# Performance work log

Measured on AMD Instinct MI355X. Metric: run time of the kernel, lower is better.

Reference implementation:

```python
import jax, jax.numpy as jnp
import numpy as np

N_NODES = 100000
N_HYPEREDGES = 50000
N_CAND = 200000
SET_SIZE = 8
EMB_DIM = 64


def setup_inputs() -> dict:
    key = jax.random.key(0)
    k1, k2, k3, k4 = jax.random.split(key, 4)
    node_emb = jax.random.normal(k1, (N_NODES, EMB_DIM), dtype=jnp.float32)
    hyperedge_emb = jax.random.normal(k2, (N_HYPEREDGES, EMB_DIM), dtype=jnp.float32)
    h = jax.random.randint(k3, (N_CAND,), 0, N_HYPEREDGES, dtype=jnp.int64)
    X = jax.random.randint(k4, (N_CAND, SET_SIZE), 0, N_NODES, dtype=jnp.int64)
    return {"node_emb": node_emb, "hyperedge_emb": hyperedge_emb, "h": h, "X": X}


def reference(node_emb, hyperedge_emb, h, X):
    # Gather per-candidate embeddings
    src = hyperedge_emb[h]          # [E, d]
    embs = node_emb[X]              # [E, S, d]

    # star_: min over nodes of sigmoid(<hyperedge, node>)
    star_scores = jax.nn.sigmoid(jnp.einsum('ed,esd->es', src, embs))  # [E, S]
    star = jnp.min(star_scores, axis=1, keepdims=True)                 # [E, 1]

    # clique_: min over all pairs of sigmoid(<node_i, node_j>)
    pair_scores = jax.nn.sigmoid(jnp.einsum('esd,etd->est', embs, embs))  # [E, S, S]
    clique = jnp.min(pair_scores, axis=(1, 2), keepdims=False)[:, None]   # [E, 1]

    return jnp.concatenate([star, clique], axis=-1)  # [E, 2]
```

## Files before the change

### kernel.cpp

```cpp
#include <hip/hip_runtime.h>
#include <hip/hip_fp16.h>
#include <math.h>
#include <float.h>

#define SET_SIZE 8
#define EMB_DIM 64
#define NPAIR 36
#define NDOT (SET_SIZE + NPAIR)

typedef _Float16 f16x2 __attribute__((ext_vector_type(2)));

union Frag32 {
    float4 f4[2];
    f16x2  h2[8];
};

__device__ __forceinline__ float dot16_f16(const Frag32& a, const Frag32& b) {
    float c = 0.0f;
#pragma unroll
    for (int j = 0; j < 8; ++j)
        c = __builtin_amdgcn_fdot2(a.h2[j], b.h2[j], c, false);
    return c;
}

__device__ __forceinline__ float quad_reduce_add(float x) {
    int t = __builtin_amdgcn_update_dpp(0, __float_as_int(x), 0xB1, 0xF, 0xF, true);
    x += __int_as_float(t);
    t = __builtin_amdgcn_update_dpp(0, __float_as_int(x), 0x4E, 0xF, 0xF, true);
    x += __int_as_float(t);
    return x;
}

__global__ __launch_bounds__(256) void cvt_both_kernel(
    const float* __restrict__ a, const float* __restrict__ b,
    __half* __restrict__ oa, __half* __restrict__ ob, int n8a, int n8b)
{
    int i = blockIdx.x * blockDim.x + threadIdx.x;
    const float* in;
    __half* out;
    int j;
    if (i < n8a) { in = a; out = oa; j = i; }
    else if (i < n8a + n8b) { in = b; out = ob; j = i - n8a; }
    else return;
    const float4* p = (const float4*)in + 2 * (size_t)j;
    float4 x = p[0], y = p[1];
    union { __half2 h2[4]; float4 f4; } u;
    u.h2[0] = __floats2half2_rn(x.x, x.y);
    u.h2[1] = __floats2half2_rn(x.z, x.w);
    u.h2[2] = __floats2half2_rn(y.x, y.y);
    u.h2[3] = __floats2half2_rn(y.z, y.w);
    ((float4*)out)[j] = u.f4;
}

__global__ __launch_bounds__(256, 5) void hyperedge_score_q4(
    const __half* __restrict__ node_f16,
    const __half* __restrict__ he_f16,
    const int*    __restrict__ h,
    const int*    __restrict__ X,
    float*        __restrict__ out,
    int n_cand)
{
    int tid = blockIdx.x * blockDim.x + threadIdx.x;
    int grp = tid >> 2;
    int q   = tid & 3;
    if (grp >= n_cand) return;

    const int4* Xv = (const int4*)(X + (size_t)grp * SET_SIZE);
    int4 x0 = Xv[0];
    int4 x1 = Xv[1];
    int he = h[grp];
    int idx[SET_SIZE] = {x0.x, x0.y, x0.z, x0.w, x1.x, x1.y, x1.z, x1.w};

    Frag32 v[9];
#pragma unroll
    for (int r = 0; r < SET_SIZE; ++r) {
        const float4* p = (const float4*)(node_f16 + (size_t)idx[r] * EMB_DIM);
        v[r].f4[0] = p[q];
        v[r].f4[1] = p[q + 4];
    }
    {
        const float4* p = (const float4*)(he_f16 + (size_t)he * EMB_DIM);
        v[8].f4[0] = p[q];
        v[8].f4[1] = p[q + 4];
    }

    float smin = FLT_MAX;
#pragma unroll
    for (int s = 0; s < SET_SIZE; ++s) {
        float d = quad_reduce_add(dot16_f16(v[8], v[s]));
        smin = fminf(smin, d);
    }

    float pmin = FLT_MAX;
#pragma unroll
    for (int s = 0; s < SET_SIZE; ++s) {
#pragma unroll
        for (int t = s; t < SET_SIZE; ++t) {
            float d = quad_reduce_add(dot16_f16(v[s], v[t]));
            pmin = fminf(pmin, d);
        }
    }

    float res = (q == 0) ? 1.0f / (1.0f + __expf(-smin))
                         : 1.0f / (1.0f + __expf(-pmin));
    if (q < 2) out[(size_t)grp * 2 + q] = res;
}

__device__ __forceinline__ float dot4f(float4 a, float4 b) {
    return fmaf(a.x, b.x, fmaf(a.y, b.y, fmaf(a.z, b.z, a.w * b.w)));
}

__global__ __launch_bounds__(256) void hyperedge_score_f32(
    const float* __restrict__ node_emb, const float* __restrict__ hyperedge_emb,
    const int* __restrict__ h, const int* __restrict__ X,
    float* __restrict__ out, int n_cand)
{
    int tid = blockIdx.x * blockDim.x + threadIdx.x;
    int grp = tid >> 3;
    int q   = tid & 7;
    if (grp >= n_cand) return;
    const int4* Xv = (const int4*)(X + (size_t)grp * SET_SIZE);
    int4 x0 = Xv[0]; int4 x1 = Xv[1];
    int he = h[grp];
    int idx[SET_SIZE] = {x0.x, x0.y, x0.z, x0.w, x1.x, x1.y, x1.z, x1.w};
    float4 va[9], vb[9];
#pragma unroll
    for (int r = 0; r < SET_SIZE; ++r) {
        const float4* p = (const float4*)(node_emb + (size_t)idx[r] * EMB_DIM) + 2 * q;
        va[r] = p[0]; vb[r] = p[1];
    }
    {
        const float4* p = (const float4*)(hyperedge_emb + (size_t)he * EMB_DIM) + 2 * q;
        va[8] = p[0]; vb[8] = p[1];
    }
    float acc[NDOT];
#pragma unroll
    for (int s = 0; s < SET_SIZE; ++s)
        acc[s] = dot4f(va[8], va[s]) + dot4f(vb[8], vb[s]);
    {
        int k = SET_SIZE;
#pragma unroll
        for (int s = 0; s < SET_SIZE; ++s)
#pragma unroll
            for (int t = s; t < SET_SIZE; ++t, ++k)
                acc[k] = dot4f(va[s], va[t]) + dot4f(vb[s], vb[t]);
    }
#pragma unroll
    for (int i = 0; i < NDOT; ++i) {
        float x = acc[i];
        x += __shfl_xor(x, 1);
        x += __shfl_xor(x, 2);
        x += __shfl_xor(x, 4);
        acc[i] = x;
    }
    float smin = acc[0];
#pragma unroll
    for (int s = 1; s < SET_SIZE; ++s) smin = fminf(smin, acc[s]);
    float pmin = acc[SET_SIZE];
#pragma unroll
    for (int i = 1; i < NPAIR; ++i) pmin = fminf(pmin, acc[SET_SIZE + i]);
    float res = (q == 0) ? 1.0f / (1.0f + __expf(-smin))
                         : 1.0f / (1.0f + __expf(-pmin));
    if (q < 2) out[(size_t)grp * 2 + q] = res;
}

extern "C" void kernel_launch(void* const* d_in, const int* in_sizes, int n_in,
                              void* d_out, int out_size, void* d_ws, size_t ws_size,
                              hipStream_t stream) {
    const float* node_emb      = (const float*)d_in[0];
    const float* hyperedge_emb = (const float*)d_in[1];
    const int*   h             = (const int*)d_in[2];
    const int*   X             = (const int*)d_in[3];
    float*       out           = (float*)d_out;

    int n_node_elems = in_sizes[0];
    int n_he_elems   = in_sizes[1];
    int n_cand       = in_sizes[2];

    size_t need = ((size_t)n_node_elems + (size_t)n_he_elems) * sizeof(__half);
    int block = 256;

    if (ws_size >= need) {
        __half* node_f16 = (__half*)d_ws;
        __half* he_f16   = node_f16 + n_node_elems;

        int n8_node = n_node_elems / 8;
        int n8_he   = n_he_elems / 8;
        int n8_tot  = n8_node + n8_he;
        cvt_both_kernel<<<(n8_tot + block - 1) / block, block, 0, stream>>>(
            node_emb, hyperedge_emb, node_f16, he_f16, n8_node, n8_he);

        long long total_threads = (long long)n_cand * 4;
        int grid_main = (int)((total_threads + block - 1) / block);
        hyperedge_score_q4<<<grid_main, block, 0, stream>>>(
            node_f16, he_f16, h, X, out, n_cand);
    } else {
        long long total_threads = (long long)n_cand * 8;
        int grid_main = (int)((total_threads + block - 1) / block);
        hyperedge_score_f32<<<grid_main, block, 0, stream>>>(
            node_emb, hyperedge_emb, h, X, out, n_cand);
    }
}
```

Before: 114.4 us.

## Grid-stride main kernel with index prefetch and nontemporal loads/stores

Turns the fp16 scoring kernel into a grid-stride loop with half as many threads, each handling two candidates. The next candidate's X and h indices are prefetched while the current one computes. Conversion loads, index loads and output stores use nontemporal hints, and the output is written as one float2 per candidate. The occupancy hint drops from 5 to 4 waves. This trades parallelism (fewer waves in flight to hide the random-gather latency) for less launch and index-fetch latency per candidate. The fp32 fallback is also restructured to reduce each dot immediately instead of keeping an accumulator array.

```diff
diff --git a/kernel.cpp b/kernel.cpp
--- a/kernel.cpp
+++ b/kernel.cpp
@@ -9,6 +9,9 @@
 #define NDOT (SET_SIZE + NPAIR)
 
 typedef _Float16 f16x2 __attribute__((ext_vector_type(2)));
+typedef float    vf4   __attribute__((ext_vector_type(4)));
+typedef float    vf2   __attribute__((ext_vector_type(2)));
+typedef int      vi4   __attribute__((ext_vector_type(4)));
 
 union Frag32 {
     float4 f4[2];
@@ -42,17 +45,18 @@
     if (i < n8a) { in = a; out = oa; j = i; }
     else if (i < n8a + n8b) { in = b; out = ob; j = i - n8a; }
     else return;
-    const float4* p = (const float4*)in + 2 * (size_t)j;
-    float4 x = p[0], y = p[1];
-    union { __half2 h2[4]; float4 f4; } u;
+    const vf4* p = (const vf4*)in + 2 * (size_t)j;
+    vf4 x = __builtin_nontemporal_load(p);
+    vf4 y = __builtin_nontemporal_load(p + 1);
+    union { __half2 h2[4]; vf4 f4; } u;
     u.h2[0] = __floats2half2_rn(x.x, x.y);
     u.h2[1] = __floats2half2_rn(x.z, x.w);
     u.h2[2] = __floats2half2_rn(y.x, y.y);
     u.h2[3] = __floats2half2_rn(y.z, y.w);
-    ((float4*)out)[j] = u.f4;
-}
-
-__global__ __launch_bounds__(256, 5) void hyperedge_score_q4(
+    ((vf4*)out)[j] = u.f4;
+}
+
+__global__ __launch_bounds__(256, 4) void hyperedge_score_q4(
     const __half* __restrict__ node_f16,
     const __half* __restrict__ he_f16,
     const int*    __restrict__ h,
@@ -60,50 +64,68 @@
     float*        __restrict__ out,
     int n_cand)
 {
-    int tid = blockIdx.x * blockDim.x + threadIdx.x;
-    int grp = tid >> 2;
-    int q   = tid & 3;
+    int tid  = blockIdx.x * blockDim.x + threadIdx.x;
+    int grp  = tid >> 2;
+    int q    = tid & 3;
+    int quads = (gridDim.x * blockDim.x) >> 2;
+
     if (grp >= n_cand) return;
 
-    const int4* Xv = (const int4*)(X + (size_t)grp * SET_SIZE);
-    int4 x0 = Xv[0];
-    int4 x1 = Xv[1];
-    int he = h[grp];
-    int idx[SET_SIZE] = {x0.x, x0.y, x0.z, x0.w, x1.x, x1.y, x1.z, x1.w};
-
-    Frag32 v[9];
-#pragma unroll
-    for (int r = 0; r < SET_SIZE; ++r) {
-        const float4* p = (const float4*)(node_f16 + (size_t)idx[r] * EMB_DIM);
-        v[r].f4[0] = p[q];
-        v[r].f4[1] = p[q + 4];
-    }
-    {
-        const float4* p = (const float4*)(he_f16 + (size_t)he * EMB_DIM);
-        v[8].f4[0] = p[q];
-        v[8].f4[1] = p[q + 4];
-    }
-
-    float smin = FLT_MAX;
-#pragma unroll
-    for (int s = 0; s < SET_SIZE; ++s) {
-        float d = quad_reduce_add(dot16_f16(v[8], v[s]));
-        smin = fminf(smin, d);
-    }
-
-    float pmin = FLT_MAX;
-#pragma unroll
-    for (int s = 0; s < SET_SIZE; ++s) {
-#pragma unroll
-        for (int t = s; t < SET_SIZE; ++t) {
-            float d = quad_reduce_add(dot16_f16(v[s], v[t]));
-            pmin = fminf(pmin, d);
-        }
-    }
-
-    float res = (q == 0) ? 1.0f / (1.0f + __expf(-smin))
-                         : 1.0f / (1.0f + __expf(-pmin));
-    if (q < 2) out[(size_t)grp * 2 + q] = res;
+    vi4 nx0 = __builtin_nontemporal_load((const vi4*)(X + (size_t)grp * SET_SIZE));
+    vi4 nx1 = __builtin_nontemporal_load((const vi4*)(X + (size_t)grp * SET_SIZE) + 1);
+    int nhe = h[grp];
+
+    for (int c = grp; c < n_cand; c += quads) {
+        vi4 x0 = nx0, x1 = nx1;
+        int he = nhe;
+        int idx[SET_SIZE] = {x0.x, x0.y, x0.z, x0.w, x1.x, x1.y, x1.z, x1.w};
+
+        Frag32 v[9];
+#pragma unroll
+        for (int r = 0; r < SET_SIZE; ++r) {
+            const float4* p = (const float4*)(node_f16 + (size_t)idx[r] * EMB_DIM);
+            v[r].f4[0] = p[q];
+            v[r].f4[1] = p[q + 4];
+        }
+        {
+            const float4* p = (const float4*)(he_f16 + (size_t)he * EMB_DIM);
+            v[8].f4[0] = p[q];
+            v[8].f4[1] = p[q + 4];
+        }
+
+        int cn = c + quads;
+        if (cn < n_cand) {
+            nx0 = __builtin_nontemporal_load((const vi4*)(X + (size_t)cn * SET_SIZE));
+            nx1 = __builtin_nontemporal_load((const vi4*)(X + (size_t)cn * SET_SIZE) + 1);
+            nhe = h[cn];
+        }
+
+        float smin = FLT_MAX;
+#pragma unroll
+        for (int s = 0; s < SET_SIZE; ++s) {
+            float d = quad_reduce_add(dot16_f16(v[8], v[s]));
+            smin = fminf(smin, d);
+        }
+
+        float pmin = FLT_MAX;
+#pragma unroll
+        for (int s = 0; s < SET_SIZE; ++s) {
+#pragma unroll
+            for (int t = s; t < SET_SIZE; ++t) {
+                float d = quad_reduce_add(dot16_f16(v[s], v[t]));
+                pmin = fminf(pmin, d);
+            }
+        }
+
+        float star_sig   = 1.0f / (1.0f + __expf(-smin));
+        float clique_sig = 1.0f / (1.0f + __expf(-pmin));
+        if (q == 0) {
+            vf2 res;
+            res.x = star_sig;
+            res.y = clique_sig;
+            __builtin_nontemporal_store(res, (vf2*)(out + (size_t)c * 2));
+        }
+    }
 }
 
 __device__ __forceinline__ float dot4f(float4 a, float4 b) {
@@ -133,32 +155,22 @@
         const float4* p = (const float4*)(hyperedge_emb + (size_t)he * EMB_DIM) + 2 * q;
         va[8] = p[0]; vb[8] = p[1];
     }
-    float acc[NDOT];
-#pragma unroll
-    for (int s = 0; s < SET_SIZE; ++s)
-        acc[s] = dot4f(va[8], va[s]) + dot4f(vb[8], vb[s]);
-    {
-        int k = SET_SIZE;
-#pragma unroll
-        for (int s = 0; s < SET_SIZE; ++s)
-#pragma unroll
-            for (int t = s; t < SET_SIZE; ++t, ++k)
-                acc[k] = dot4f(va[s], va[t]) + dot4f(vb[s], vb[t]);
-    }
-#pragma unroll
-    for (int i = 0; i < NDOT; ++i) {
-        float x = acc[i];
-        x += __shfl_xor(x, 1);
-        x += __shfl_xor(x, 2);
-        x += __shfl_xor(x, 4);
-        acc[i] = x;
-    }
-    float smin = acc[0];
-#pragma unroll
-    for (int s = 1; s < SET_SIZE; ++s) smin = fminf(smin, acc[s]);
-    float pmin = acc[SET_SIZE];
-#pragma unroll
-    for (int i = 1; i < NPAIR; ++i) pmin = fminf(pmin, acc[SET_SIZE + i]);
+    float smin = FLT_MAX, pmin = FLT_MAX;
+#pragma unroll
+    for (int s = 0; s < SET_SIZE; ++s) {
+        float x = dot4f(va[8], va[s]) + dot4f(vb[8], vb[s]);
+        x += __shfl_xor(x, 1); x += __shfl_xor(x, 2); x += __shfl_xor(x, 4);
+        smin = fminf(smin, x);
+    }
+#pragma unroll
+    for (int s = 0; s < SET_SIZE; ++s) {
+#pragma unroll
+        for (int t = s; t < SET_SIZE; ++t) {
+            float x = dot4f(va[s], va[t]) + dot4f(vb[s], vb[t]);
+            x += __shfl_xor(x, 1); x += __shfl_xor(x, 2); x += __shfl_xor(x, 4);
+            pmin = fminf(pmin, x);
+        }
+    }
     float res = (q == 0) ? 1.0f / (1.0f + __expf(-smin))
                          : 1.0f / (1.0f + __expf(-pmin));
     if (q < 2) out[(size_t)grp * 2 + q] = res;
@@ -190,7 +202,8 @@
         cvt_both_kernel<<<(n8_tot + block - 1) / block, block, 0, stream>>>(
             node_emb, hyperedge_emb, node_f16, he_f16, n8_node, n8_he);
 
-        long long total_threads = (long long)n_cand * 4;
+        const int UNROLL = 2;
+        long long total_threads = ((long long)n_cand * 4 + UNROLL - 1) / UNROLL;
         int grid_main = (int)((total_threads + block - 1) / block);
         hyperedge_score_q4<<<grid_main, block, 0, stream>>>(
             node_f16, he_f16, h, X, out, n_cand);
```

Measured after the change: 118.3 us. +3.4%, slower.
